# Performance work log

Measured on AMD Instinct MI355X. Metric: run time of the kernel, lower is better.

Reference implementation:

```python
import jax, jax.numpy as jnp
import numpy as np

N_NODES = 50000
N_EDGES = 1600000
LORA_R = 8


def gcn_conv(h, W, b, src, dst, n):
    # PyG GCNConv: linear transform, add self-loops, symmetric normalization,
    # scatter-add aggregation at target nodes, then bias.
    h = h @ W  # [N, out]
    ones = jnp.ones(src.shape[0], dtype=h.dtype)
    deg = jax.ops.segment_sum(ones, dst, num_segments=n) + 1.0  # +1 for self-loop
    dis = jax.lax.rsqrt(deg)  # deg >= 1 always
    norm = dis[src] * dis[dst]  # [E]
    agg = jax.ops.segment_sum(norm[:, None] * h[src], dst, num_segments=n)
    agg = agg + (dis * dis)[:, None] * h  # self-loop contribution
    return agg + b


def lora(h, A, B):
    # LoRALinear: b(a(x)) * (1/r); replaces input (not additive)
    return (h @ A) @ B * (1.0 / LORA_R)


def setup_inputs() -> dict:
    key = jax.random.key(0)
    ks = jax.random.split(key, 12)
    inp = {}
    inp['x'] = jax.random.normal(ks[0], (N_NODES, 128), dtype=jnp.float32)
    inp['edge_index'] = jax.random.randint(ks[1], (2, N_EDGES), 0, N_NODES, dtype=jnp.int64 if jax.config.jax_enable_x64 else jnp.int32)
    inp['domain_idx'] = jax.random.randint(ks[2], (N_NODES,), 0, 3, dtype=jnp.int32)
    inp['emb_table'] = jax.random.normal(ks[3], (3, 4096), dtype=jnp.float32)
    s1 = 1.0 / np.sqrt(4224.0)
    inp['W1'] = jax.random.normal(ks[4], (4224, 32), dtype=jnp.float32) * s1
    inp['b1'] = jnp.zeros((32,), dtype=jnp.float32)
    inp['A1'] = jax.random.normal(ks[5], (32, LORA_R), dtype=jnp.float32) * (1.0 / np.sqrt(32.0))
    inp['B1'] = jax.random.normal(ks[6], (LORA_R, 32), dtype=jnp.float32) * (1.0 / np.sqrt(LORA_R))
    inp['W2'] = jax.random.normal(ks[7], (32, 5), dtype=jnp.float32) * (1.0 / np.sqrt(32.0))
    inp['b2'] = jnp.zeros((5,), dtype=jnp.float32)
    inp['A2'] = jax.random.normal(ks[8], (5, LORA_R), dtype=jnp.float32) * (1.0 / np.sqrt(5.0))
    inp['B2'] = jax.random.normal(ks[9], (LORA_R, 5), dtype=jnp.float32) * (1.0 / np.sqrt(LORA_R))
    return inp


def reference(x, edge_index, domain_idx, emb_table, W1, b1, A1, B1, W2, b2, A2, B2):
    n = x.shape[0]
    src, dst = edge_index[0], edge_index[1]
    embedded = emb_table[domain_idx]  # [N, 4096]
    h = jnp.concatenate([embedded, x], axis=1)  # [N, 4224]
    h = gcn_conv(h, W1, b1, src, dst, n)
    h = lora(h, A1, B1)
    h = jax.nn.relu(h)
    h = gcn_conv(h, W2, b2, src, dst, n)
    h = lora(h, A2, B2)
    return jax.nn.log_softmax(h, axis=1)
```

## Files before the change

### kernel.cpp

```cpp
#include <hip/hip_runtime.h>
#include <hip/hip_bf16.h>
#include <hip/hip_fp16.h>


#define XDIM 128
#define EMBDIM 4096
#define TB 4096
#define BSH 6
#define BN 64
#define ECAP2 2560
#define POISON 0xAAAAAAAAu
#define BCSH 5

__global__ void __launch_bounds__(256) kA(
    const int* __restrict__ src, const int* __restrict__ dst,
    unsigned int* __restrict__ sorted, unsigned int* __restrict__ bcur,
    int e, int ntiles,
    const float* __restrict__ emb, const float* __restrict__ W1,
    float* __restrict__ emb_part,
    const float* __restrict__ A1, const float* __restrict__ A2,
    const float* __restrict__ B2, const float* __restrict__ b1,
    float* __restrict__ M2, float* __restrict__ b1A1,
    const float* __restrict__ x, float* __restrict__ g, int n) {
    __shared__ __align__(16) char smem[24576];
    int t = threadIdx.x, bx = blockIdx.x;
    if (bx < ntiles) {
        unsigned int* staged = (unsigned int*)smem;
        int* loff = (int*)(smem + 16384);
        int* rctr = (int*)(smem + 20480);
        int base = bx * TB;
        int len = min(TB, e - base);
        for (int i = t; i < 1024; i += 256) { loff[i] = 0; rctr[i] = 0; }
        __syncthreads();
        for (int i = t; i < len; i += 256) atomicAdd(&loff[dst[base + i] >> BSH], 1);
        __syncthreads();
        if (t < 64) {
            int ch = t * 16;
            int v[16]; int s0 = 0;
            #pragma unroll
            for (int k = 0; k < 16; ++k) { v[k] = loff[ch + k]; s0 += v[k]; }
            int pre = s0;
            #pragma unroll
            for (int d2 = 1; d2 < 64; d2 <<= 1) {
                int up = __shfl_up(pre, d2);
                if (t >= d2) pre += up;
            }
            int excl = pre - s0;
            #pragma unroll
            for (int k = 0; k < 16; ++k) { loff[ch + k] = excl; excl += v[k]; }
        }
        __syncthreads();
        for (int i = t; i < len; i += 256) {
            int s = src[base + i], d = dst[base + i];
            int b = d >> BSH;
            int r = atomicAdd(&rctr[b], 1);
            staged[loff[b] + r] = ((unsigned int)d << 16) | (unsigned int)s;
        }
        __syncthreads();
        for (int b2 = t; b2 < 1024; b2 += 256) {
            int l = rctr[b2];
            if (l > 0) rctr[b2] = (int)(atomicAdd(&bcur[b2 << BCSH], (unsigned)l) - POISON);
        }
        __syncthreads();
        for (int i = t; i < len; i += 256) {
            unsigned int u = staged[i];
            int b2 = (int)(u >> 22);
            int pos = rctr[b2] + (i - loff[b2]);
            if (pos < ECAP2) sorted[(size_t)b2 * ECAP2 + pos] = u;
        }
    } else if (bx < ntiles + 96) {
        float* red = (float*)smem;
        int bx2 = bx - ntiles;
        int dm = bx2 >> 5, seg = bx2 & 31;
        const float* er = emb + dm * EMBDIM + seg * 128;
        const float* wr = W1 + (size_t)(seg * 128) * 32;
        int j = t & 31, kk = t >> 5;
        float acc = 0.f;
        for (int k2 = kk; k2 < 128; k2 += 8) acc += er[k2] * wr[k2 * 32 + j];
        red[kk * 32 + j] = acc;
        __syncthreads();
        if (t < 32) {
            float s = 0.f;
            #pragma unroll
            for (int r = 0; r < 8; ++r) s += red[r * 32 + t];
            emb_part[bx2 * 32 + t] = s;
        }
        if (bx2 == 0) {
            if (t < 25) {
                int c = t / 5, cp = t % 5;
                float s = 0.f;
                #pragma unroll
                for (int r = 0; r < 8; ++r) s += A2[c * 8 + r] * B2[r * 5 + cp];
                M2[c * 5 + cp] = s * 0.125f;
            }
            if (t >= 32 && t < 40) {
                int j2 = t - 32;
                float s = 0.f;
                #pragma unroll
                for (int k = 0; k < 32; ++k) s += b1[k] * A1[k * 8 + j2];
                b1A1[j2] = s;
            }
        }
    } else {
        __half* xsh = (__half*)smem;
        float* sWA  = (float*)(smem + 16384);
        float* sA1  = (float*)(smem + 20480);
        int gb = bx - ntiles - 96;
        int row0 = gb * 64;
        sA1[t] = A1[t];
        for (int i = t; i < 2048; i += 256) {
            int row = i >> 5, c4 = i & 31;
            int gi = row0 + row;
            float4 v = (gi < n) ? ((const float4*)x)[(size_t)gi * 32 + c4]
                                : make_float4(0.f, 0.f, 0.f, 0.f);
            __half2 h01 = __floats2half2_rn(v.x, v.y);
            __half2 h23 = __floats2half2_rn(v.z, v.w);
            uint2 pk;
            pk.x = *(unsigned int*)&h01;
            pk.y = *(unsigned int*)&h23;
            *(uint2*)(xsh + row * 128 + c4 * 4) = pk;
        }
        __syncthreads();
        for (int idx = t; idx < 1024; idx += 256) {
            int k = idx >> 3, j = idx & 7;
            const float* wr = W1 + (size_t)(EMBDIM + k) * 32;
            float s = 0.f;
            #pragma unroll 8
            for (int c = 0; c < 32; ++c) s += wr[c] * sA1[c * 8 + j];
            sWA[idx] = s;
        }
        __syncthreads();
        int row = t >> 3, j = t & 7;
        const __half2* xr1 = (const __half2*)(xsh + row * 128);
        const __half2* xr2 = (const __half2*)(xsh + (row + 32) * 128);
        float acc1 = 0.f, acc2 = 0.f;
        #pragma unroll 8
        for (int k2 = 0; k2 < 64; ++k2) {
            float2 fa = __half22float2(xr1[k2]);
            float2 fb = __half22float2(xr2[k2]);
            float w0 = sWA[(2 * k2) * 8 + j];
            float w1 = sWA[(2 * k2 + 1) * 8 + j];
            acc1 += fa.x * w0 + fa.y * w1;
            acc2 += fb.x * w0 + fb.y * w1;
        }
        int gi1 = row0 + row, gi2 = row0 + row + 32;
        if (gi1 < n) g[(size_t)gi1 * 8 + j] = acc1;
        if (gi2 < n) g[(size_t)gi2 * 8 + j] = acc2;
    }
}

__global__ void __launch_bounds__(256) kB(
    const unsigned int* __restrict__ sorted, const unsigned int* __restrict__ bcur,
    const float* __restrict__ emb_part, const float* __restrict__ A1,
    const int* __restrict__ dom, const float* __restrict__ g,
    int* __restrict__ deg, __half* __restrict__ p1h,
    unsigned short* __restrict__ nsrc, int n) {
    __shared__ int hist[64], eoff[64], rctr[64], sdom[64];
    __shared__ float sA1[256], sproj[96], sembA1[24];
    __shared__ __align__(16) unsigned short esrc[ECAP2];
    int t = threadIdx.x, b = blockIdx.x;
    int row0 = b << BSH;
    if (t < 64) {
        hist[t] = 0; rctr[t] = 0;
        int gi = row0 + t;
        sdom[t] = (gi < n) ? dom[gi] : 0;
    }
    sA1[t] = A1[t];
    if (t < 96) {
        int dm = t >> 5, c = t & 31;
        float s = 0.f;
        #pragma unroll
        for (int seg = 0; seg < 32; ++seg) s += emb_part[(dm * 32 + seg) * 32 + c];
        sproj[dm * 32 + c] = s;
    }
    __syncthreads();
    int m = (int)(bcur[b << BCSH] - POISON);
    if (m > ECAP2) m = ECAP2;
    const unsigned int* sp = sorted + (size_t)b * ECAP2;
    for (int i = t; i < m; i += 256) atomicAdd(&hist[(sp[i] >> 16) & (BN - 1)], 1);
    __syncthreads();
    if (t < 64) {
        int v = hist[t];
        int pre = v;
        #pragma unroll
        for (int d2 = 1; d2 < 64; d2 <<= 1) {
            int up = __shfl_up(pre, d2);
            if (t >= d2) pre += up;
        }
        eoff[t] = pre - v;
        int gi = row0 + t;
        if (gi < n) deg[gi] = v;
    } else if (t < 88) {
        int dm = (t - 64) >> 3, j = (t - 64) & 7;
        float s = 0.f;
        #pragma unroll 8
        for (int c = 0; c < 32; ++c) s += sproj[dm * 32 + c] * sA1[c * 8 + j];
        sembA1[dm * 8 + j] = s;
    }
    __syncthreads();
    for (int i = t; i < m; i += 256) {
        unsigned int u = sp[i];
        int dl = (int)(u >> 16) & (BN - 1);
        int r = atomicAdd(&rctr[dl], 1);
        esrc[eoff[dl] + r] = (unsigned short)(u & 0xffffu);
    }
    for (int i = t; i < 512; i += 256) {
        int row = i >> 3, j = i & 7;
        int gi = row0 + row;
        if (gi < n) {
            float dd = rsqrtf((float)(hist[row] + 1));
            float v = g[(size_t)gi * 8 + j] + sembA1[sdom[row] * 8 + j];
            p1h[(size_t)gi * 8 + j] = __float2half_rn(dd * v);
        }
    }
    __syncthreads();
    {
        uint4* npw = (uint4*)(nsrc + (size_t)b * ECAP2);
        const uint4* ew = (const uint4*)esrc;
        int mw = (m + 7) >> 3;
        for (int i = t; i < mw; i += 256) npw[i] = ew[i];
    }
}

__global__ void __launch_bounds__(256) k_bagg1(
    const __half* __restrict__ p1h, const unsigned short* __restrict__ nsrc,
    const unsigned int* __restrict__ bcur, const int* __restrict__ deg,
    const float* __restrict__ b1A1, const float* __restrict__ B1,
    const float* __restrict__ W2, __half* __restrict__ qh, int n) {
    __shared__ __align__(16) unsigned short esrc[ECAP2];
    __shared__ int eoff[BN], sdeg[BN];
    __shared__ float pacc[3][BN][8];
    __shared__ float sB1[256], sW2[160], sb[8];
    int t = threadIdx.x, b = blockIdx.x;
    int node0 = b << BSH;
    sB1[t] = B1[t];
    if (t < 160) sW2[t] = W2[t];
    if (t < 8) sb[t] = b1A1[t];
    if (t < 64) {
        int node = node0 + t;
        int v = (node < n) ? deg[node] : 0;
        sdeg[t] = v;
        int pre = v;
        #pragma unroll
        for (int d2 = 1; d2 < 64; d2 <<= 1) {
            int up = __shfl_up(pre, d2);
            if (t >= d2) pre += up;
        }
        eoff[t] = pre - v;
    }
    __syncthreads();
    int m = (int)(bcur[b << BCSH] - POISON);
    if (m > ECAP2) m = ECAP2;
    {
        const uint4* npw = (const uint4*)(nsrc + (size_t)b * ECAP2);
        uint4* ew = (uint4*)esrc;
        int mw = (m + 7) >> 3;
        for (int i = t; i < mw; i += 256) ew[i] = npw[i];
    }
    __syncthreads();
    int nodeL = t & (BN - 1), tsub = t >> BSH;
    int base0 = eoff[nodeL], c = sdeg[nodeL];
    float a[8] = {0.f, 0.f, 0.f, 0.f, 0.f, 0.f, 0.f, 0.f};
    float a2[8] = {0.f, 0.f, 0.f, 0.f, 0.f, 0.f, 0.f, 0.f};
    int k = tsub;
    for (; k + 4 < c; k += 8) {
        int s1 = esrc[base0 + k], s2 = esrc[base0 + k + 4];
        uint4 u = *(const uint4*)(p1h + (size_t)s1 * 8);
        uint4 v = *(const uint4*)(p1h + (size_t)s2 * 8);
        float2 f;
        f = __half22float2(*(__half2*)&u.x); a[0] += f.x; a[1] += f.y;
        f = __half22float2(*(__half2*)&u.y); a[2] += f.x; a[3] += f.y;
        f = __half22float2(*(__half2*)&u.z); a[4] += f.x; a[5] += f.y;
        f = __half22float2(*(__half2*)&u.w); a[6] += f.x; a[7] += f.y;
        f = __half22float2(*(__half2*)&v.x); a2[0] += f.x; a2[1] += f.y;
        f = __half22float2(*(__half2*)&v.y); a2[2] += f.x; a2[3] += f.y;
        f = __half22float2(*(__half2*)&v.z); a2[4] += f.x; a2[5] += f.y;
        f = __half22float2(*(__half2*)&v.w); a2[6] += f.x; a2[7] += f.y;
    }
    for (; k < c; k += 4) {
        int s1 = esrc[base0 + k];
        uint4 u = *(const uint4*)(p1h + (size_t)s1 * 8);
        float2 f;
        f = __half22float2(*(__half2*)&u.x); a[0] += f.x; a[1] += f.y;
        f = __half22float2(*(__half2*)&u.y); a[2] += f.x; a[3] += f.y;
        f = __half22float2(*(__half2*)&u.z); a[4] += f.x; a[5] += f.y;
        f = __half22float2(*(__half2*)&u.w); a[6] += f.x; a[7] += f.y;
    }
    #pragma unroll
    for (int j = 0; j < 8; ++j) a[j] += a2[j];
    if (tsub > 0) {
        #pragma unroll
        for (int j = 0; j < 8; ++j) pacc[tsub - 1][nodeL][j] = a[j];
    }
    __syncthreads();
    if (t < BN) {
        int node = node0 + t;
        if (node < n) {
            float dd = rsqrtf((float)(sdeg[t] + 1));
            uint4 u = *(const uint4*)(p1h + (size_t)node * 8);
            float2 f;
            float af[8];
            f = __half22float2(*(__half2*)&u.x); af[0] = a[0] + f.x; af[1] = a[1] + f.y;
            f = __half22float2(*(__half2*)&u.y); af[2] = a[2] + f.x; af[3] = a[3] + f.y;
            f = __half22float2(*(__half2*)&u.z); af[4] = a[4] + f.x; af[5] = a[5] + f.y;
            f = __half22float2(*(__half2*)&u.w); af[6] = a[6] + f.x; af[7] = a[7] + f.y;
            #pragma unroll
            for (int ps = 0; ps < 3; ++ps) {
                #pragma unroll
                for (int j = 0; j < 8; ++j) af[j] += pacc[ps][t][j];
            }
            #pragma unroll
            for (int j = 0; j < 8; ++j) af[j] = dd * af[j] + sb[j];
            float qv[5] = {0.f, 0.f, 0.f, 0.f, 0.f};
            #pragma unroll
            for (int c2 = 0; c2 < 32; ++c2) {
                float tv = 0.f;
                #pragma unroll
                for (int j = 0; j < 8; ++j) tv += af[j] * sB1[j * 32 + c2];
                float st = fmaxf(tv * 0.125f, 0.f);
                #pragma unroll
                for (int o = 0; o < 5; ++o) qv[o] += st * sW2[c2 * 5 + o];
            }
            #pragma unroll
            for (int o = 0; o < 5; ++o) qh[(size_t)node * 8 + o] = __float2half_rn(dd * qv[o]);
        }
    }
}

__global__ void __launch_bounds__(256) k_bagg2(
    const __half* __restrict__ qh, const unsigned short* __restrict__ nsrc,
    const unsigned int* __restrict__ bcur, const int* __restrict__ deg,
    const float* __restrict__ b2, const float* __restrict__ M2,
    float* __restrict__ out, int n) {
    __shared__ __align__(16) unsigned short esrc[ECAP2];
    __shared__ int eoff[BN], sdeg[BN];
    __shared__ float pacc[3][BN][5];
    __shared__ float sM2[25], sb2[5];
    int t = threadIdx.x, b = blockIdx.x;
    int node0 = b << BSH;
    if (t < 25) sM2[t] = M2[t];
    if (t < 5) sb2[t] = b2[t];
    if (t < 64) {
        int node = node0 + t;
        int v = (node < n) ? deg[node] : 0;
        sdeg[t] = v;
        int pre = v;
        #pragma unroll
        for (int d2 = 1; d2 < 64; d2 <<= 1) {
            int up = __shfl_up(pre, d2);
            if (t >= d2) pre += up;
        }
        eoff[t] = pre - v;
    }
    __syncthreads();
    int m = (int)(bcur[b << BCSH] - POISON);
    if (m > ECAP2) m = ECAP2;
    {
        const uint4* npw = (const uint4*)(nsrc + (size_t)b * ECAP2);
        uint4* ew = (uint4*)esrc;
        int mw = (m + 7) >> 3;
        for (int i = t; i < mw; i += 256) ew[i] = npw[i];
    }
    __syncthreads();
    int nodeL = t & (BN - 1), tsub = t >> BSH;
    int base0 = eoff[nodeL], c = sdeg[nodeL];
    float a[5] = {0.f, 0.f, 0.f, 0.f, 0.f};
    float a2[5] = {0.f, 0.f, 0.f, 0.f, 0.f};
    int k = tsub;
    for (; k + 4 < c; k += 8) {
        int s1 = esrc[base0 + k], s2 = esrc[base0 + k + 4];
        uint4 u = *(const uint4*)(qh + (size_t)s1 * 8);
        uint4 v = *(const uint4*)(qh + (size_t)s2 * 8);
        float2 f;
        f = __half22float2(*(__half2*)&u.x); a[0] += f.x; a[1] += f.y;
        f = __half22float2(*(__half2*)&u.y); a[2] += f.x; a[3] += f.y;
        f = __half22float2(*(__half2*)&u.z); a[4] += f.x;
        f = __half22float2(*(__half2*)&v.x); a2[0] += f.x; a2[1] += f.y;
        f = __half22float2(*(__half2*)&v.y); a2[2] += f.x; a2[3] += f.y;
        f = __half22float2(*(__half2*)&v.z); a2[4] += f.x;
    }
    for (; k < c; k += 4) {
        int s1 = esrc[base0 + k];
        uint4 u = *(const uint4*)(qh + (size_t)s1 * 8);
        float2 f;
        f = __half22float2(*(__half2*)&u.x); a[0] += f.x; a[1] += f.y;
        f = __half22float2(*(__half2*)&u.y); a[2] += f.x; a[3] += f.y;
        f = __half22float2(*(__half2*)&u.z); a[4] += f.x;
    }
    #pragma unroll
    for (int j = 0; j < 5; ++j) a[j] += a2[j];
    if (tsub > 0) {
        #pragma unroll
        for (int j = 0; j < 5; ++j) pacc[tsub - 1][nodeL][j] = a[j];
    }
    __syncthreads();
    if (t < BN) {
        int node = node0 + t;
        if (node < n) {
            float dd = rsqrtf((float)(sdeg[t] + 1));
            uint4 u = *(const uint4*)(qh + (size_t)node * 8);
            float2 f;
            float av[5];
            f = __half22float2(*(__half2*)&u.x); av[0] = a[0] + f.x; av[1] = a[1] + f.y;
            f = __half22float2(*(__half2*)&u.y); av[2] = a[2] + f.x; av[3] = a[3] + f.y;
            f = __half22float2(*(__half2*)&u.z); av[4] = a[4] + f.x;
            #pragma unroll
            for (int ps = 0; ps < 3; ++ps) {
                #pragma unroll
                for (int j = 0; j < 5; ++j) av[j] += pacc[ps][t][j];
            }
            #pragma unroll
            for (int j = 0; j < 5; ++j) av[j] = dd * av[j] + sb2[j];
            float z[5];
            #pragma unroll
            for (int cp = 0; cp < 5; ++cp) {
                float s = 0.f;
                #pragma unroll
                for (int c2 = 0; c2 < 5; ++c2) s += av[c2] * sM2[c2 * 5 + cp];
                z[cp] = s;
            }
            float mx = z[0];
            #pragma unroll
            for (int c2 = 1; c2 < 5; ++c2) mx = fmaxf(mx, z[c2]);
            float ssum = 0.f;
            #pragma unroll
            for (int c2 = 0; c2 < 5; ++c2) ssum += __expf(z[c2] - mx);
            float ls = __logf(ssum);
            #pragma unroll
            for (int c2 = 0; c2 < 5; ++c2) out[node * 5 + c2] = z[c2] - mx - ls;
        }
    }
}

extern "C" void kernel_launch(void* const* d_in, const int* in_sizes, int n_in,
                              void* d_out, int out_size, void* d_ws, size_t ws_size,
                              hipStream_t stream) {
    const float* x   = (const float*)d_in[0];
    const int*   ei  = (const int*)d_in[1];
    const int*   dom = (const int*)d_in[2];
    const float* emb = (const float*)d_in[3];
    const float* W1  = (const float*)d_in[4];
    const float* b1  = (const float*)d_in[5];
    const float* A1  = (const float*)d_in[6];
    const float* B1  = (const float*)d_in[7];
    const float* W2  = (const float*)d_in[8];
    const float* b2  = (const float*)d_in[9];
    const float* A2  = (const float*)d_in[10];
    const float* B2  = (const float*)d_in[11];
    float* out = (float*)d_out;

    int n = in_sizes[2];
    int e = in_sizes[1] / 2;
    const int* src = ei;
    const int* dst = ei + e;

    int ntiles = (e + TB - 1) / TB;
    int nbuck  = (n + BN - 1) >> BSH;
    int ngb    = (n + 63) / 64;

    char* base = (char*)d_ws;
    size_t o = 0;
    auto carve = [&](size_t bytes) {
        void* p = base + o;
        o = (o + bytes + 15) & ~(size_t)15;
        return p;
    };
    float* emb_part = (float*)carve(96 * 32 * sizeof(float));
    float* M2       = (float*)carve(32 * sizeof(float));
    float* b1A1     = (float*)carve(8 * sizeof(float));
    unsigned int* bcur = (unsigned int*)carve((size_t)1024 * 32 * sizeof(int));
    int*   deg      = (int*)carve((size_t)n * sizeof(int));
    float* g        = (float*)carve((size_t)n * 8 * sizeof(float));
    __half* p1h     = (__half*)carve((size_t)n * 8 * sizeof(__half));
    __half* qh      = (__half*)carve((size_t)n * 8 * sizeof(__half));
    unsigned int* sorted = (unsigned int*)carve((size_t)nbuck * ECAP2 * sizeof(unsigned int));
    unsigned short* nsrc = (unsigned short*)carve((size_t)nbuck * ECAP2 * sizeof(unsigned short));
    (void)ws_size; (void)n_in; (void)out_size;

    kA<<<ntiles + 96 + ngb, 256, 0, stream>>>(
        src, dst, sorted, bcur, e, ntiles,
        emb, W1, emb_part, A1, A2, B2, b1, M2, b1A1, x, g, n);
    kB<<<nbuck, 256, 0, stream>>>(sorted, bcur, emb_part, A1, dom, g,
                                  deg, p1h, nsrc, n);
    k_bagg1<<<nbuck, 256, 0, stream>>>(p1h, nsrc, bcur, deg, b1A1, B1, W2, qh, n);
    k_bagg2<<<nbuck, 256, 0, stream>>>(qh, nsrc, bcur, deg, b2, M2, out, n);
}
```

Before: 154.3 us.

## Scatter edges directly to global buckets and halve x-projection rows per block

The edge-bucketing path drops the shared-memory staging buffer and the exclusive prefix scan. Each tile now reserves its global bucket offsets right after the histogram and scatters edges straight into the sorted array using per-bucket shared atomics. That cuts shared memory from 24KB to 16KB and removes two passes and barriers, which should raise occupancy. The cost is that global writes are no longer grouped contiguously by bucket within a tile, so coalescing gets worse. The x-projection blocks now handle 32 rows instead of 64, which doubles the number of blocks and recomputes the WA product in each block.

```diff
diff --git a/kernel.cpp b/kernel.cpp
--- a/kernel.cpp
+++ b/kernel.cpp
@@ -22,51 +22,29 @@
     const float* __restrict__ B2, const float* __restrict__ b1,
     float* __restrict__ M2, float* __restrict__ b1A1,
     const float* __restrict__ x, float* __restrict__ g, int n) {
-    __shared__ __align__(16) char smem[24576];
+    __shared__ __align__(16) char smem[16384];
     int t = threadIdx.x, bx = blockIdx.x;
     if (bx < ntiles) {
-        unsigned int* staged = (unsigned int*)smem;
-        int* loff = (int*)(smem + 16384);
-        int* rctr = (int*)(smem + 20480);
+        int* loff = (int*)smem;
+        int* rctr = (int*)(smem + 4096);
         int base = bx * TB;
         int len = min(TB, e - base);
         for (int i = t; i < 1024; i += 256) { loff[i] = 0; rctr[i] = 0; }
         __syncthreads();
         for (int i = t; i < len; i += 256) atomicAdd(&loff[dst[base + i] >> BSH], 1);
         __syncthreads();
-        if (t < 64) {
-            int ch = t * 16;
-            int v[16]; int s0 = 0;
-            #pragma unroll
-            for (int k = 0; k < 16; ++k) { v[k] = loff[ch + k]; s0 += v[k]; }
-            int pre = s0;
-            #pragma unroll
-            for (int d2 = 1; d2 < 64; d2 <<= 1) {
-                int up = __shfl_up(pre, d2);
-                if (t >= d2) pre += up;
-            }
-            int excl = pre - s0;
-            #pragma unroll
-            for (int k = 0; k < 16; ++k) { loff[ch + k] = excl; excl += v[k]; }
+        for (int b2 = t; b2 < 1024; b2 += 256) {
+            int l = loff[b2];
+            if (l > 0) loff[b2] = (int)(atomicAdd(&bcur[b2 << BCSH], (unsigned)l) - POISON);
         }
         __syncthreads();
         for (int i = t; i < len; i += 256) {
             int s = src[base + i], d = dst[base + i];
-            int b = d >> BSH;
-            int r = atomicAdd(&rctr[b], 1);
-            staged[loff[b] + r] = ((unsigned int)d << 16) | (unsigned int)s;
-        }
-        __syncthreads();
-        for (int b2 = t; b2 < 1024; b2 += 256) {
-            int l = rctr[b2];
-            if (l > 0) rctr[b2] = (int)(atomicAdd(&bcur[b2 << BCSH], (unsigned)l) - POISON);
-        }
-        __syncthreads();
-        for (int i = t; i < len; i += 256) {
-            unsigned int u = staged[i];
-            int b2 = (int)(u >> 22);
-            int pos = rctr[b2] + (i - loff[b2]);
-            if (pos < ECAP2) sorted[(size_t)b2 * ECAP2 + pos] = u;
+            int b2 = d >> BSH;
+            int r = atomicAdd(&rctr[b2], 1);
+            int pos = loff[b2] + r;
+            if (pos < ECAP2)
+                sorted[(size_t)b2 * ECAP2 + pos] = ((unsigned int)d << 16) | (unsigned int)s;
         }
     } else if (bx < ntiles + 96) {
         float* red = (float*)smem;
@@ -103,12 +81,12 @@
         }
     } else {
         __half* xsh = (__half*)smem;
-        float* sWA  = (float*)(smem + 16384);
-        float* sA1  = (float*)(smem + 20480);
+        float* sWA  = (float*)(smem + 8192);
+        float* sA1  = (float*)(smem + 12288);
         int gb = bx - ntiles - 96;
-        int row0 = gb * 64;
+        int row0 = gb * 32;
         sA1[t] = A1[t];
-        for (int i = t; i < 2048; i += 256) {
+        for (int i = t; i < 1024; i += 256) {
             int row = i >> 5, c4 = i & 31;
             int gi = row0 + row;
             float4 v = (gi < n) ? ((const float4*)x)[(size_t)gi * 32 + c4]
@@ -132,20 +110,16 @@
         __syncthreads();
         int row = t >> 3, j = t & 7;
         const __half2* xr1 = (const __half2*)(xsh + row * 128);
-        const __half2* xr2 = (const __half2*)(xsh + (row + 32) * 128);
-        float acc1 = 0.f, acc2 = 0.f;
+        float acc1 = 0.f;
         #pragma unroll 8
         for (int k2 = 0; k2 < 64; ++k2) {
             float2 fa = __half22float2(xr1[k2]);
-            float2 fb = __half22float2(xr2[k2]);
             float w0 = sWA[(2 * k2) * 8 + j];
             float w1 = sWA[(2 * k2 + 1) * 8 + j];
             acc1 += fa.x * w0 + fa.y * w1;
-            acc2 += fb.x * w0 + fb.y * w1;
-        }
-        int gi1 = row0 + row, gi2 = row0 + row + 32;
+        }
+        int gi1 = row0 + row;
         if (gi1 < n) g[(size_t)gi1 * 8 + j] = acc1;
-        if (gi2 < n) g[(size_t)gi2 * 8 + j] = acc2;
     }
 }
 
@@ -456,7 +430,7 @@
 
     int ntiles = (e + TB - 1) / TB;
     int nbuck  = (n + BN - 1) >> BSH;
-    int ngb    = (n + 63) / 64;
+    int ngb    = (n + 31) / 32;
 
     char* base = (char*)d_ws;
     size_t o = 0;
```

Measured after the change: 161.7 us. 1.05x slower.
